# Optimization experiments

Hardware: AMD Instinct MI355X
Metric: run time of the kernel (lower is better)

The kernel has to match this reference:

```python
import jax, jax.numpy as jnp
import numpy as np

BN_EPS = 1e-5
RENORM_EPS = 1e-9


def setup_inputs() -> dict:
    key = jax.random.key(0)
    ks = jax.random.split(key, 8)
    B, C, N = 4, 256, 4096
    D = C // 4
    return {
        "x": jax.random.normal(ks[0], (B, C, N), jnp.float32),
        "y": jax.random.normal(ks[1], (B, C, N), jnp.float32),
        "w_qkx": jax.random.normal(ks[2], (D, C), jnp.float32) / np.sqrt(C),
        "w_vx": jax.random.normal(ks[3], (C, C), jnp.float32) / np.sqrt(C),
        "w_tx": jax.random.normal(ks[4], (C, C), jnp.float32) / np.sqrt(C),
        "w_qky": jax.random.normal(ks[5], (D, C), jnp.float32) / np.sqrt(C),
        "w_vy": jax.random.normal(ks[6], (C, C), jnp.float32) / np.sqrt(C),
        "w_ty": jax.random.normal(ks[7], (C, C), jnp.float32) / np.sqrt(C),
        "gamma": jnp.ones((C,), jnp.float32),
        "beta": jnp.zeros((C,), jnp.float32),
    }


def _conv1x1(w, x):
    # w: (O, C), x: (B, C, N) -> (B, O, N)
    return jnp.einsum("oc,bcn->bon", w, x)


def _batchnorm1d(x, gamma, beta):
    # training-mode BN over (B, N) per channel, biased variance (torch default)
    mean = x.mean(axis=(0, 2), keepdims=True)
    var = ((x - mean) ** 2).mean(axis=(0, 2), keepdims=True)
    xhat = (x - mean) * jax.lax.rsqrt(var + BN_EPS)
    return gamma[None, :, None] * xhat + beta[None, :, None]


def _branch(src, tgt, w_qk, w_v, w_t, gamma, beta):
    # cross-attention: queries from tgt, keys/values from src; output length = len(tgt)
    q = _conv1x1(w_qk, tgt)          # (B, D, M)
    k = _conv1x1(w_qk, src)          # (B, D, N)
    v = _conv1x1(w_v, src)           # (B, C, N)
    energy = jnp.einsum("bdm,bdn->bmn", q, k)      # (B, M, N)
    att = jax.nn.softmax(energy, axis=-1)
    att = att / (RENORM_EPS + att.sum(axis=2, keepdims=True))  # extra L1 renorm
    r = jnp.einsum("bcn,bmn->bcm", v, att)         # (B, C, M)
    return jax.nn.relu(_batchnorm1d(_conv1x1(w_t, r), gamma, beta))


def reference(x, y, w_qkx, w_vx, w_tx, w_qky, w_vy, w_ty, gamma, beta):
    r_x = _branch(x, y, w_qkx, w_vx, w_tx, gamma, beta)  # queries from y, kv from x
    r_y = _branch(y, x, w_qky, w_vy, w_ty, gamma, beta)  # queries from x, kv from y
    return (x + r_x, y + r_y)
```

## Files before the change

kernel.cpp:

```cpp
#include <hip/hip_runtime.h>

constexpr int Bc = 4;
constexpr int Cc = 256;
constexpr int Dc = 64;
constexpr int Nc = 4096;

typedef __attribute__((ext_vector_type(8))) _Float16 f16x8;
typedef __attribute__((ext_vector_type(4))) _Float16 f16x4;
typedef __attribute__((ext_vector_type(4))) float f32x4;

__device__ inline float exp2fast(float x) { return __builtin_amdgcn_exp2f(x); }

__device__ inline void gload_lds16(const _Float16* g, _Float16* lds) {
  __builtin_amdgcn_global_load_lds(
      (const __attribute__((address_space(1))) unsigned int*)g,
      (__attribute__((address_space(3))) unsigned int*)lds, 16, 0, 0);
}

__global__ __launch_bounds__(256) void wconv_kernel(
    const float* __restrict__ Wvx, const float* __restrict__ Wvy,
    const float* __restrict__ Wtx, const float* __restrict__ Wty,
    const float* __restrict__ Wqkx, const float* __restrict__ Wqky,
    _Float16* __restrict__ Wh)
{
  const int i = blockIdx.x * 256 + threadIdx.x;
  const int z = blockIdx.y;
  if (z < 4) {
    const float* w = (z == 0) ? Wvx : (z == 1) ? Wvy : (z == 2) ? Wtx : Wty;
    Wh[(size_t)z * Cc * Cc + i] = (_Float16)w[i];
  } else if (i < Dc * Cc) {
    const float* w = (z == 4) ? Wqkx : Wqky;
    Wh[(size_t)4 * Cc * Cc + (size_t)(z - 4) * Dc * Cc + i] = (_Float16)w[i];
  }
}

__global__ __launch_bounds__(256) void transpose_kernel(
    const float* __restrict__ X, const float* __restrict__ Y,
    _Float16* __restrict__ Xt)
{
  __shared__ float tile[64][65];
  const int t  = threadIdx.x;
  const int n0 = blockIdx.x * 64;
  const int c0 = blockIdx.y * 64;
  const int z  = blockIdx.z, br = z >> 2, b = z & 3;
  const float* In = (br ? Y : X) + (size_t)b * Cc * Nc;
#pragma unroll
  for (int p = 0; p < 4; ++p) {
    const int c = p * 16 + (t >> 4), n4 = (t & 15) * 4;
    float4 v = *(const float4*)&In[(size_t)(c0 + c) * Nc + n0 + n4];
    tile[c][n4 + 0] = v.x; tile[c][n4 + 1] = v.y;
    tile[c][n4 + 2] = v.z; tile[c][n4 + 3] = v.w;
  }
  __syncthreads();
  _Float16* Ob = Xt + ((size_t)(br * Bc + b) * Nc + n0) * Cc + c0;
#pragma unroll
  for (int p = 0; p < 4; ++p) {
    const int n = p * 16 + (t >> 4), c4 = (t & 15) * 4;
    f16x4 w;
#pragma unroll
    for (int j = 0; j < 4; ++j) w[j] = (_Float16)tile[c4 + j][n];
    *(f16x4*)&Ob[(size_t)n * Cc + c4] = w;
  }
}

__global__ __launch_bounds__(256, 4) void conv_qk_mfma_kernel(
    const _Float16* __restrict__ Xt, const _Float16* __restrict__ Wh,
    _Float16* __restrict__ Qt, _Float16* __restrict__ Kt)
{
  const int t  = threadIdx.x;
  const int ws = t >> 6, l = t & 63, lr = l & 15, lg = l >> 4;
  const int n_w = blockIdx.x * 128 + ws * 32;
  const int qk = blockIdx.y;
  const int z  = blockIdx.z, br = z >> 2, b = z & 3;
  const size_t bb = (size_t)(br * Bc + b);
  const int insel = (qk ^ br ^ 1) & 1;
  _Float16* Out = qk ? Kt : Qt;
  const float scale = qk ? 1.0f : 1.44269504088896f;

  const _Float16* wbase = Wh + (size_t)4 * Cc * Cc + (size_t)br * Dc * Cc
                          + (size_t)lr * Cc + lg * 8;
  const _Float16* xbase = Xt + ((size_t)(insel * Bc + b) * Nc + n_w + lr) * Cc + lg * 8;

  f32x4 acc[4][2] = {};
  for (int c0 = 0; c0 < Cc; c0 += 32) {
    f16x8 wf[4], xf[2];
#pragma unroll
    for (int dt = 0; dt < 4; ++dt)
      wf[dt] = *(const f16x8*)(wbase + (size_t)(dt * 16) * Cc + c0);
#pragma unroll
    for (int nt = 0; nt < 2; ++nt)
      xf[nt] = *(const f16x8*)(xbase + (size_t)(nt * 16) * Cc + c0);
#pragma unroll
    for (int dt = 0; dt < 4; ++dt)
#pragma unroll
      for (int nt = 0; nt < 2; ++nt)
        acc[dt][nt] = __builtin_amdgcn_mfma_f32_16x16x32_f16(wf[dt], xf[nt], acc[dt][nt], 0, 0, 0);
  }
#pragma unroll
  for (int dt = 0; dt < 4; ++dt)
#pragma unroll
    for (int nt = 0; nt < 2; ++nt) {
      const int n  = n_w + nt * 16 + lr;
      const int d0 = dt * 16 + lg * 4;
      const int off = qk ? (d0 ^ ((n & 7) << 3)) : d0;
      f16x4 o4;
#pragma unroll
      for (int r = 0; r < 4; ++r) o4[r] = (_Float16)(acc[dt][nt][r] * scale);
      *(f16x4*)&Out[(bb * Nc + n) * 64 + off] = o4;
    }
}

__global__ __launch_bounds__(256, 4) void conv_v_mfma_kernel(
    const _Float16* __restrict__ Xt, const _Float16* __restrict__ Wh,
    _Float16* __restrict__ Vb)
{
  const int t  = threadIdx.x;
  const int ws = t >> 6, l = t & 63, lr = l & 15, lg = l >> 4;
  const int wm = ws >> 1, wo = ws & 1;
  const int n_w = blockIdx.x * 128 + wm * 64;
  const int o_w = blockIdx.y * 128 + wo * 64;
  const int z  = blockIdx.z, br = z >> 2, b = z & 3;
  const size_t bb = (size_t)(br * Bc + b);

  const _Float16* abase = Xt + (bb * Nc + n_w + lr) * Cc + lg * 8;
  const _Float16* bbase = Wh + ((size_t)br * Cc + o_w + lr) * Cc + lg * 8;
  f32x4 acc[4][4] = {};

  for (int c0 = 0; c0 < Cc; c0 += 32) {
    f16x8 af[4], bfr[4];
#pragma unroll
    for (int mt = 0; mt < 4; ++mt)
      af[mt] = *(const f16x8*)(abase + (size_t)(mt * 16) * Cc + c0);
#pragma unroll
    for (int ot = 0; ot < 4; ++ot)
      bfr[ot] = *(const f16x8*)(bbase + (size_t)(ot * 16) * Cc + c0);
#pragma unroll
    for (int ot = 0; ot < 4; ++ot)
#pragma unroll
      for (int mt = 0; mt < 4; ++mt)
        acc[ot][mt] = __builtin_amdgcn_mfma_f32_16x16x32_f16(af[mt], bfr[ot], acc[ot][mt], 0, 0, 0);
  }
#pragma unroll
  for (int ot = 0; ot < 4; ++ot)
#pragma unroll
    for (int mt = 0; mt < 4; ++mt) {
      const int cout = o_w + ot * 16 + lr;
      const int n = n_w + mt * 16 + lg * 4;
      f16x4 o4;
#pragma unroll
      for (int r = 0; r < 4; ++r) o4[r] = (_Float16)acc[ot][mt][r];
      *(f16x4*)&Vb[(bb * Cc + cout) * Nc + n] = o4;
    }
}

__global__ __launch_bounds__(768, 3) void attn_mfma_kernel(
    const _Float16* __restrict__ Qt,
    const _Float16* __restrict__ Kt,
    const _Float16* __restrict__ V,
    _Float16* __restrict__ Op,
    float* __restrict__ Ml,
    int nsp, int kn)
{
  __shared__ __align__(16) _Float16 k_lds[2][64 * 64];
  __shared__ __align__(16) _Float16 p_lds[2][64 * 64];
  __shared__ float s_fac[2][64];

  const int t  = threadIdx.x;
  const int ws = t >> 6;
  const int l  = t & 63;
  const int lr = l & 15;
  const int lg = l >> 4;

  const int nwg  = (Nc / 64) * nsp * 8;
  const int lin  = blockIdx.x + gridDim.x * (blockIdx.y + gridDim.y * blockIdx.z);
  const int work = (lin & 7) * (nwg >> 3) + (lin >> 3);
  const int m0   = (work & 63) * 64;
  const int spbb = work >> 6;
  const int sp   = spbb % nsp;
  const size_t bb = (size_t)(spbb / nsp);

  const _Float16* kgl = Kt + (bb * Nc + (size_t)sp * kn) * 64;
  const int nch = kn >> 6;

  if (ws < 4) {
    const _Float16* qp = Qt + (bb * Nc + m0 + ws * 16 + lr) * 64 + lg * 8;
    const f16x8 qf0 = *(const f16x8*)qp;
    const f16x8 qf1 = *(const f16x8*)(qp + 32);
    const _Float16* gq = kgl + ws * 512 + l * 8;

    float m_run = -1e30f, l_run = 0.f;
    const int mrow = ws * 16 + lr;
    const int sw   = (mrow & 7) << 4;

    {
#pragma unroll
      for (int r = 0; r < 2; ++r)
        gload_lds16(gq + r * 2048, &k_lds[0][ws * 512 + r * 2048]);
    }
    __syncthreads();

    for (int ch2 = 0; ch2 < nch; ch2 += 2) {
#pragma unroll
      for (int par = 0; par < 2; ++par) {
        const int ch = ch2 + par;
        if (ch + 1 < nch) {
          const _Float16* g = gq + (size_t)(ch + 1) * (64 * 64);
#pragma unroll
          for (int r = 0; r < 2; ++r)
            gload_lds16(g + r * 2048, &k_lds[par ^ 1][ws * 512 + r * 2048]);
        }
        f32x4 st[4] = {};
#pragma unroll
        for (int nt = 0; nt < 4; ++nt) {
          const int   krow = nt * 16 + lr;
          const char* krp  = (const char*)&k_lds[par][krow * 64];
          const int   swr  = (krow & 7) << 4;
          f16x8 kh0 = *(const f16x8*)(krp + ((lg * 16) ^ swr));
          f16x8 kh1 = *(const f16x8*)(krp + ((64 + lg * 16) ^ swr));
          st[nt] = __builtin_amdgcn_mfma_f32_16x16x32_f16(kh0, qf0, st[nt], 0, 0, 0);
          st[nt] = __builtin_amdgcn_mfma_f32_16x16x32_f16(kh1, qf1, st[nt], 0, 0, 0);
        }
        float mx = st[0][0];
#pragma unroll
        for (int nt = 0; nt < 4; ++nt)
#pragma unroll
          for (int rr = 0; rr < 4; ++rr) mx = fmaxf(mx, st[nt][rr]);
        float s = 1.0f;
        if (__any(mx > m_run + 12.0f)) {
          mx = fmaxf(mx, __shfl_xor(mx, 16));
          mx = fmaxf(mx, __shfl_xor(mx, 32));
          const float mnew = fmaxf(m_run, mx);
          s = exp2fast(m_run - mnew);
          m_run = mnew;
        }
        float sum = 0.f;
        float p[4][4];
#pragma unroll
        for (int nt = 0; nt < 4; ++nt)
#pragma unroll
          for (int rr = 0; rr < 4; ++rr) {
            p[nt][rr] = exp2fast(st[nt][rr] - m_run);
            sum += p[nt][rr];
          }
        l_run = l_run * s + sum;
        {
          char* prow = (char*)&p_lds[par][mrow * 64];
#pragma unroll
          for (int nt = 0; nt < 4; ++nt) {
            f16x4 pb;
            pb[0] = (_Float16)p[nt][0]; pb[1] = (_Float16)p[nt][1];
            pb[2] = (_Float16)p[nt][2]; pb[3] = (_Float16)p[nt][3];
            *(f16x4*)(prow + ((nt * 32 + lg * 8) ^ sw)) = pb;
          }
        }
        if (lg == 0) s_fac[par][ws * 16 + lr] = s;
        __syncthreads();
      }
    }

    l_run += __shfl_xor(l_run, 16);
    l_run += __shfl_xor(l_run, 32);
    if (lg == 0) {
      size_t mi = ((bb * nsp + sp) * Nc + m0 + ws * 16 + lr) * 2;
      Ml[mi]     = m_run;
      Ml[mi + 1] = l_run;
    }
  } else {
    const int cw = ws - 4;
    const _Float16* vbase = V + (bb * Cc + cw * 32 + lr) * Nc + sp * kn + lg * 8;
    f32x4 acc[2][4] = {};
    f16x8 vf[2][2][2];

    __syncthreads();

    for (int ch2 = 0; ch2 < nch; ch2 += 2) {
#pragma unroll
      for (int par = 0; par < 2; ++par) {
        const int ch = ch2 + par;
        {
          const _Float16* vp = vbase + ch * 64;
#pragma unroll
          for (int ct = 0; ct < 2; ++ct)
#pragma unroll
            for (int kk = 0; kk < 2; ++kk)
              vf[par][ct][kk] = *(const f16x8*)(vp + (size_t)ct * 16 * Nc + kk * 32);
        }
        if (ch > 0) {
          float scm[4];
#pragma unroll
          for (int mt = 0; mt < 4; ++mt) scm[mt] = s_fac[par ^ 1][mt * 16 + lr];
          const int needs = (scm[0] != 1.f) | (scm[1] != 1.f) |
                            (scm[2] != 1.f) | (scm[3] != 1.f);
          if (__any(needs)) {
#pragma unroll
            for (int ct = 0; ct < 2; ++ct)
#pragma unroll
              for (int mt = 0; mt < 4; ++mt) {
                acc[ct][mt][0] *= scm[mt]; acc[ct][mt][1] *= scm[mt];
                acc[ct][mt][2] *= scm[mt]; acc[ct][mt][3] *= scm[mt];
              }
          }
          f16x8 pf[4][2];
#pragma unroll
          for (int mt = 0; mt < 4; ++mt) {
            const int   rm  = mt * 16 + lr;
            const char* pr  = (const char*)&p_lds[par ^ 1][rm * 64];
            const int   swr = (rm & 7) << 4;
#pragma unroll
            for (int kk = 0; kk < 2; ++kk)
              pf[mt][kk] = *(const f16x8*)(pr + ((lg * 16 + kk * 64) ^ swr));
          }
          __builtin_amdgcn_s_setprio(1);
#pragma unroll
          for (int ct = 0; ct < 2; ++ct)
#pragma unroll
            for (int kk = 0; kk < 2; ++kk)
#pragma unroll
              for (int mt = 0; mt < 4; ++mt)
                acc[ct][mt] = __builtin_amdgcn_mfma_f32_16x16x32_f16(vf[par ^ 1][ct][kk], pf[mt][kk], acc[ct][mt], 0, 0, 0);
          __builtin_amdgcn_s_setprio(0);
        }
        __syncthreads();
      }
    }

    {
      float scm[4];
#pragma unroll
      for (int mt = 0; mt < 4; ++mt) scm[mt] = s_fac[1][mt * 16 + lr];
      const int needs = (scm[0] != 1.f) | (scm[1] != 1.f) |
                        (scm[2] != 1.f) | (scm[3] != 1.f);
      if (__any(needs)) {
#pragma unroll
        for (int ct = 0; ct < 2; ++ct)
#pragma unroll
          for (int mt = 0; mt < 4; ++mt) {
            acc[ct][mt][0] *= scm[mt]; acc[ct][mt][1] *= scm[mt];
            acc[ct][mt][2] *= scm[mt]; acc[ct][mt][3] *= scm[mt];
          }
      }
      f16x8 pf[4][2];
#pragma unroll
      for (int mt = 0; mt < 4; ++mt) {
        const int   rm  = mt * 16 + lr;
        const char* pr  = (const char*)&p_lds[1][rm * 64];
        const int   swr = (rm & 7) << 4;
#pragma unroll
        for (int kk = 0; kk < 2; ++kk)
          pf[mt][kk] = *(const f16x8*)(pr + ((lg * 16 + kk * 64) ^ swr));
      }
#pragma unroll
      for (int ct = 0; ct < 2; ++ct)
#pragma unroll
        for (int kk = 0; kk < 2; ++kk)
#pragma unroll
          for (int mt = 0; mt < 4; ++mt)
            acc[ct][mt] = __builtin_amdgcn_mfma_f32_16x16x32_f16(vf[1][ct][kk], pf[mt][kk], acc[ct][mt], 0, 0, 0);
    }

    _Float16* ob = Op + (bb * nsp + sp) * (size_t)Cc * Nc;
#pragma unroll
    for (int ct = 0; ct < 2; ++ct)
#pragma unroll
      for (int mt = 0; mt < 4; ++mt) {
        const int c0 = cw * 32 + ct * 16 + lg * 4;
        const int m  = m0 + mt * 16 + lr;
        f16x4 o4;
#pragma unroll
        for (int r = 0; r < 4; ++r) o4[r] = (_Float16)acc[ct][mt][r];
        *(f16x4*)&ob[(size_t)m * Cc + c0] = o4;
      }
  }
}

__global__ __launch_bounds__(256) void combine_kernel(
    const _Float16* __restrict__ Op, const float* __restrict__ Ml,
    _Float16* __restrict__ Rt, int nsp)
{
  const int tid = blockIdx.x * 256 + threadIdx.x;
  const int c0 = (tid & 63) * 4;
  const int m  = (tid >> 6) & (Nc - 1);
  const int bb = tid >> 18;
  float val[4];
  if (nsp == 2) {
    const _Float16* o0 = Op + ((size_t)bb * 2 + 0) * Cc * Nc + (size_t)m * Cc + c0;
    const _Float16* o1 = Op + ((size_t)bb * 2 + 1) * Cc * Nc + (size_t)m * Cc + c0;
    const float* ml0 = Ml + (((size_t)bb * 2 + 0) * Nc + m) * 2;
    const float* ml1 = Ml + (((size_t)bb * 2 + 1) * Nc + m) * 2;
    float m1 = ml0[0], L1 = ml0[1], m2 = ml1[0], L2 = ml1[1];
    float M  = fmaxf(m1, m2);
    float w1 = __builtin_amdgcn_exp2f(m1 - M), w2 = __builtin_amdgcn_exp2f(m2 - M);
    float inv = 1.0f / (w1 * L1 + w2 * L2);
    f16x4 a = *(const f16x4*)o0;
    f16x4 d = *(const f16x4*)o1;
#pragma unroll
    for (int j = 0; j < 4; ++j) val[j] = (w1 * (float)a[j] + w2 * (float)d[j]) * inv;
  } else {
    const _Float16* o0 = Op + (size_t)bb * Cc * Nc + (size_t)m * Cc + c0;
    const float* ml0 = Ml + ((size_t)bb * Nc + m) * 2;
    float inv = 1.0f / ml0[1];
    f16x4 a = *(const f16x4*)o0;
#pragma unroll
    for (int j = 0; j < 4; ++j) val[j] = (float)a[j] * inv;
  }
  f16x4 r4;
#pragma unroll
  for (int j = 0; j < 4; ++j) r4[j] = (_Float16)val[j];
  *(f16x4*)&Rt[((size_t)bb * Nc + m) * Cc + c0] = r4;
}

__global__ __launch_bounds__(256, 4) void conv_t_mfma_kernel(
    const _Float16* __restrict__ Rt, const _Float16* __restrict__ Wh,
    _Float16* __restrict__ Th, float* __restrict__ part)
{
  __shared__ float red[2][2][4][16][2];
  const int t  = threadIdx.x;
  const int ws = t >> 6, l = t & 63, lr = l & 15, lg = l >> 4;
  const int wm = ws >> 1, wo = ws & 1;
  const int m_w = blockIdx.x * 128 + wm * 64;
  const int o_w = blockIdx.y * 128 + wo * 64;
  const int z  = blockIdx.z, br = z >> 2, b = z & 3;
  const size_t bb = (size_t)(br * Bc + b);

  const _Float16* abase = Rt + (bb * Nc + m_w + lr) * Cc + lg * 8;
  const _Float16* bbase = Wh + ((size_t)(2 + br) * Cc + o_w + lr) * Cc + lg * 8;
  f32x4 acc[4][4] = {};

  for (int c0 = 0; c0 < Cc; c0 += 32) {
    f16x8 af[4], bfr[4];
#pragma unroll
    for (int mt = 0; mt < 4; ++mt)
      af[mt] = *(const f16x8*)(abase + (size_t)(mt * 16) * Cc + c0);
#pragma unroll
    for (int ot = 0; ot < 4; ++ot)
      bfr[ot] = *(const f16x8*)(bbase + (size_t)(ot * 16) * Cc + c0);
#pragma unroll
    for (int ot = 0; ot < 4; ++ot)
#pragma unroll
      for (int mt = 0; mt < 4; ++mt)
        acc[ot][mt] = __builtin_amdgcn_mfma_f32_16x16x32_f16(af[mt], bfr[ot], acc[ot][mt], 0, 0, 0);
  }
  _Float16* Tb = Th + bb * Cc * Nc;
#pragma unroll
  for (int ot = 0; ot < 4; ++ot) {
    float s = 0.f, q = 0.f;
#pragma unroll
    for (int mt = 0; mt < 4; ++mt) {
      const int o = o_w + ot * 16 + lr;
      const int m = m_w + mt * 16 + lg * 4;
      f16x4 h4;
#pragma unroll
      for (int r = 0; r < 4; ++r) {
        float v = acc[ot][mt][r];
        h4[r] = (_Float16)v;
        s += v; q += v * v;
      }
      *(f16x4*)&Tb[(size_t)o * Nc + m] = h4;
    }
    s += __shfl_xor(s, 16); s += __shfl_xor(s, 32);
    q += __shfl_xor(q, 16); q += __shfl_xor(q, 32);
    if (lg == 0) { red[wm][wo][ot][lr][0] = s; red[wm][wo][ot][lr][1] = q; }
  }
  __syncthreads();
  {
    const int wo2 = t >> 7, ot2 = (t >> 5) & 3, lr2 = (t >> 1) & 15, kind = t & 1;
    float v = red[0][wo2][ot2][lr2][kind] + red[1][wo2][ot2][lr2][kind];
    const int c = blockIdx.y * 128 + wo2 * 64 + ot2 * 16 + lr2;
    const int slot = blockIdx.x * 4 + b;
    part[(((size_t)br * Cc + c) * 128 + slot) * 2 + kind] = v;
  }
}

__global__ __launch_bounds__(256) void bn_finalize_kernel(
    const float* __restrict__ part, float* __restrict__ stats)
{
  const int br = blockIdx.x, c = threadIdx.x;
  const float* p = part + ((size_t)br * Cc + c) * 128 * 2;
  float s = 0.f, q = 0.f;
#pragma unroll 4
  for (int i = 0; i < 128; ++i) { s += p[i * 2]; q += p[i * 2 + 1]; }
  const float inv_n = 1.0f / (float)(Bc * Nc);
  const float mean = s * inv_n;
  const float var  = q * inv_n - mean * mean;
  stats[(br * 2 + 0) * Cc + c] = mean;
  stats[(br * 2 + 1) * Cc + c] = rsqrtf(var + 1e-5f);
}

__global__ __launch_bounds__(256) void bn_out_kernel(
    const _Float16* __restrict__ Th, float* __restrict__ OUT,
    const float* __restrict__ X, const float* __restrict__ Y,
    const float* __restrict__ stats, const float* __restrict__ gamma,
    const float* __restrict__ beta)
{
  const int br = blockIdx.y;
  const int i = blockIdx.x * 256 + threadIdx.x;
  const size_t flat = ((size_t)i << 2);
  const int c = (int)((flat >> 12) & (Cc - 1));
  float mean = stats[(br * 2 + 0) * Cc + c], istd = stats[(br * 2 + 1) * Cc + c];
  float gm = gamma[c], bt = beta[c];
  const _Float16* Tb = Th + (size_t)br * Bc * Cc * Nc;
  float* Ob = OUT + (size_t)br * Bc * Cc * Nc;
  const float* SRC = (br ? Y : X);
  f16x4 t4 = *(const f16x4*)&Tb[flat];
  float4 s4 = *(const float4*)&SRC[flat];
  float4 o4;
  o4.x = s4.x + fmaxf(0.f, gm * ((float)t4[0] - mean) * istd + bt);
  o4.y = s4.y + fmaxf(0.f, gm * ((float)t4[1] - mean) * istd + bt);
  o4.z = s4.z + fmaxf(0.f, gm * ((float)t4[2] - mean) * istd + bt);
  o4.w = s4.w + fmaxf(0.f, gm * ((float)t4[3] - mean) * istd + bt);
  *(float4*)&Ob[flat] = o4;
}

extern "C" void kernel_launch(void* const* d_in, const int* in_sizes, int n_in,
                              void* d_out, int out_size, void* d_ws, size_t ws_size,
                              hipStream_t stream) {
  const float* x     = (const float*)d_in[0];
  const float* y     = (const float*)d_in[1];
  const float* w_qkx = (const float*)d_in[2];
  const float* w_vx  = (const float*)d_in[3];
  const float* w_tx  = (const float*)d_in[4];
  const float* w_qky = (const float*)d_in[5];
  const float* w_vy  = (const float*)d_in[6];
  const float* w_ty  = (const float*)d_in[7];
  const float* gamma = (const float*)d_in[8];
  const float* beta  = (const float*)d_in[9];

  float* out = (float*)d_out;

  const int nsp = (ws_size >= 60ull * 1024 * 1024) ? 2 : 1;
  const int kn  = Nc / nsp;

  char* wsb = (char*)d_ws;
  _Float16* qt = (_Float16*)wsb;
  _Float16* kt = (_Float16*)(wsb + (4ull << 20));
  _Float16* vb = (_Float16*)(wsb + (8ull << 20));
  _Float16* xt = (_Float16*)(wsb + (24ull << 20));
  _Float16* op = (_Float16*)(wsb + (24ull << 20));
  size_t off = (24ull << 20) + (size_t)nsp * (16ull << 20);
  float* ml = (float*)(wsb + off);
  off += (size_t)nsp * (256ull << 10);
  _Float16* wh = (_Float16*)(wsb + off);
  off += (640ull << 10);
  float* part = (float*)(wsb + off);
  off += (512ull << 10);
  float* st = (float*)(wsb + off);
  _Float16* rt = (_Float16*)wsb;
  _Float16* th = (_Float16*)(wsb + (24ull << 20));

  wconv_kernel<<<dim3(Cc * Cc / 256, 6), 256, 0, stream>>>(w_vx, w_vy, w_tx, w_ty, w_qkx, w_qky, wh);
  transpose_kernel<<<dim3(Nc / 64, Cc / 64, 8), 256, 0, stream>>>(x, y, xt);
  conv_qk_mfma_kernel<<<dim3(Nc / 128, 2, 8), 256, 0, stream>>>(xt, wh, qt, kt);
  conv_v_mfma_kernel<<<dim3(Nc / 128, Cc / 128, 8), 256, 0, stream>>>(xt, wh, vb);
  attn_mfma_kernel<<<dim3(Nc / 64, nsp, 8), 768, 0, stream>>>(qt, kt, vb, op, ml, nsp, kn);
  combine_kernel<<<(2 * Bc * Nc * (Cc / 4)) / 256, 256, 0, stream>>>(op, ml, rt, nsp);
  conv_t_mfma_kernel<<<dim3(Nc / 128, Cc / 128, 8), 256, 0, stream>>>(rt, wh, th, part);
  bn_finalize_kernel<<<2, 256, 0, stream>>>(part, st);
  bn_out_kernel<<<dim3((Bc * Cc * Nc / 4) / 256, 2), 256, 0, stream>>>(th, out, x, y, st, gamma, beta);
}
```

Baseline: 244.6 us.

## Triple-buffer K tiles with prefetch depth two and manual barriers

After: 266.8 us. 1.09x slower.

```diff
diff --git a/kernel.cpp b/kernel.cpp
--- a/kernel.cpp
+++ b/kernel.cpp
@@ -161,7 +161,7 @@
     float* __restrict__ Ml,
     int nsp, int kn)
 {
-  __shared__ __align__(16) _Float16 k_lds[2][64 * 64];
+  __shared__ __align__(16) _Float16 k_lds[3][64 * 64];
   __shared__ __align__(16) _Float16 p_lds[2][64 * 64];
   __shared__ float s_fac[2][64];
 
@@ -196,66 +196,79 @@
 #pragma unroll
       for (int r = 0; r < 2; ++r)
         gload_lds16(gq + r * 2048, &k_lds[0][ws * 512 + r * 2048]);
-    }
-    __syncthreads();
-
-    for (int ch2 = 0; ch2 < nch; ch2 += 2) {
-#pragma unroll
-      for (int par = 0; par < 2; ++par) {
-        const int ch = ch2 + par;
-        if (ch + 1 < nch) {
-          const _Float16* g = gq + (size_t)(ch + 1) * (64 * 64);
-#pragma unroll
-          for (int r = 0; r < 2; ++r)
-            gload_lds16(g + r * 2048, &k_lds[par ^ 1][ws * 512 + r * 2048]);
+#pragma unroll
+      for (int r = 0; r < 2; ++r)
+        gload_lds16(gq + (64 * 64) + r * 2048, &k_lds[1][ws * 512 + r * 2048]);
+      asm volatile("s_waitcnt vmcnt(2)" ::: "memory");
+    }
+    __builtin_amdgcn_s_barrier();
+    __builtin_amdgcn_sched_barrier(0);
+
+    int cur = 0;
+    for (int ch = 0; ch < nch; ++ch) {
+      const int par = ch & 1;
+      const bool more = (ch + 2 < nch);
+      if (more) {
+        int stg = cur + 2; if (stg >= 3) stg -= 3;
+        const _Float16* g = gq + (size_t)(ch + 2) * (64 * 64);
+#pragma unroll
+        for (int r = 0; r < 2; ++r)
+          gload_lds16(g + r * 2048, &k_lds[stg][ws * 512 + r * 2048]);
+      }
+      const _Float16* kbuf = &k_lds[cur][0];
+      f32x4 st[4] = {};
+#pragma unroll
+      for (int nt = 0; nt < 4; ++nt) {
+        const int   krow = nt * 16 + lr;
+        const char* krp  = (const char*)(kbuf + krow * 64);
+        const int   swr  = (krow & 7) << 4;
+        f16x8 kh0 = *(const f16x8*)(krp + ((lg * 16) ^ swr));
+        f16x8 kh1 = *(const f16x8*)(krp + ((64 + lg * 16) ^ swr));
+        st[nt] = __builtin_amdgcn_mfma_f32_16x16x32_f16(kh0, qf0, st[nt], 0, 0, 0);
+        st[nt] = __builtin_amdgcn_mfma_f32_16x16x32_f16(kh1, qf1, st[nt], 0, 0, 0);
+      }
+      float mx = st[0][0];
+#pragma unroll
+      for (int nt = 0; nt < 4; ++nt)
+#pragma unroll
+        for (int rr = 0; rr < 4; ++rr) mx = fmaxf(mx, st[nt][rr]);
+      float s = 1.0f;
+      if (__any(mx > m_run + 12.0f)) {
+        mx = fmaxf(mx, __shfl_xor(mx, 16));
+        mx = fmaxf(mx, __shfl_xor(mx, 32));
+        const float mnew = fmaxf(m_run, mx);
+        s = exp2fast(m_run - mnew);
+        m_run = mnew;
+      }
+      float sum = 0.f;
+      float p[4][4];
+#pragma unroll
+      for (int nt = 0; nt < 4; ++nt)
+#pragma unroll
+        for (int rr = 0; rr < 4; ++rr) {
+          p[nt][rr] = exp2fast(st[nt][rr] - m_run);
+          sum += p[nt][rr];
         }
-        f32x4 st[4] = {};
+      l_run = l_run * s + sum;
+      {
+        char* prow = (char*)&p_lds[par][mrow * 64];
 #pragma unroll
         for (int nt = 0; nt < 4; ++nt) {
-          const int   krow = nt * 16 + lr;
-          const char* krp  = (const char*)&k_lds[par][krow * 64];
-          const int   swr  = (krow & 7) << 4;
-          f16x8 kh0 = *(const f16x8*)(krp + ((lg * 16) ^ swr));
-          f16x8 kh1 = *(const f16x8*)(krp + ((64 + lg * 16) ^ swr));
-          st[nt] = __builtin_amdgcn_mfma_f32_16x16x32_f16(kh0, qf0, st[nt], 0, 0, 0);
-          st[nt] = __builtin_amdgcn_mfma_f32_16x16x32_f16(kh1, qf1, st[nt], 0, 0, 0);
+          f16x4 pb;
+          pb[0] = (_Float16)p[nt][0]; pb[1] = (_Float16)p[nt][1];
+          pb[2] = (_Float16)p[nt][2]; pb[3] = (_Float16)p[nt][3];
+          *(f16x4*)(prow + ((nt * 32 + lg * 8) ^ sw)) = pb;
         }
-        float mx = st[0][0];
-#pragma unroll
-        for (int nt = 0; nt < 4; ++nt)
-#pragma unroll
-          for (int rr = 0; rr < 4; ++rr) mx = fmaxf(mx, st[nt][rr]);
-        float s = 1.0f;
-        if (__any(mx > m_run + 12.0f)) {
-          mx = fmaxf(mx, __shfl_xor(mx, 16));
-          mx = fmaxf(mx, __shfl_xor(mx, 32));
-          const float mnew = fmaxf(m_run, mx);
-          s = exp2fast(m_run - mnew);
-          m_run = mnew;
-        }
-        float sum = 0.f;
-        float p[4][4];
-#pragma unroll
-        for (int nt = 0; nt < 4; ++nt)
-#pragma unroll
-          for (int rr = 0; rr < 4; ++rr) {
-            p[nt][rr] = exp2fast(st[nt][rr] - m_run);
-            sum += p[nt][rr];
-          }
-        l_run = l_run * s + sum;
-        {
-          char* prow = (char*)&p_lds[par][mrow * 64];
-#pragma unroll
-          for (int nt = 0; nt < 4; ++nt) {
-            f16x4 pb;
-            pb[0] = (_Float16)p[nt][0]; pb[1] = (_Float16)p[nt][1];
-            pb[2] = (_Float16)p[nt][2]; pb[3] = (_Float16)p[nt][3];
-            *(f16x4*)(prow + ((nt * 32 + lg * 8) ^ sw)) = pb;
-          }
-        }
-        if (lg == 0) s_fac[par][ws * 16 + lr] = s;
-        __syncthreads();
-      }
+      }
+      if (lg == 0) s_fac[par][ws * 16 + lr] = s;
+      if (more) {
+        asm volatile("s_waitcnt vmcnt(2) lgkmcnt(0)" ::: "memory");
+      } else {
+        asm volatile("s_waitcnt vmcnt(0) lgkmcnt(0)" ::: "memory");
+      }
+      __builtin_amdgcn_s_barrier();
+      __builtin_amdgcn_sched_barrier(0);
+      cur = (cur + 1 == 3) ? 0 : cur + 1;
     }
 
     l_run += __shfl_xor(l_run, 16);
@@ -271,7 +284,8 @@
     f32x4 acc[2][4] = {};
     f16x8 vf[2][2][2];
 
-    __syncthreads();
+    __builtin_amdgcn_s_barrier();
+    __builtin_amdgcn_sched_barrier(0);
 
     for (int ch2 = 0; ch2 < nch; ch2 += 2) {
 #pragma unroll
@@ -320,7 +334,9 @@
                 acc[ct][mt] = __builtin_amdgcn_mfma_f32_16x16x32_f16(vf[par ^ 1][ct][kk], pf[mt][kk], acc[ct][mt], 0, 0, 0);
           __builtin_amdgcn_s_setprio(0);
         }
-        __syncthreads();
+        asm volatile("s_waitcnt lgkmcnt(0)" ::: "memory");
+        __builtin_amdgcn_s_barrier();
+        __builtin_amdgcn_sched_barrier(0);
       }
     }
 
```

## Drop split-K attention and fuse softmax normalization into attention epilogue

Applied to the files above, without the earlier changes.

After: 230.4 us. -5.8%, faster.

```diff
diff --git a/kernel.cpp b/kernel.cpp
--- a/kernel.cpp
+++ b/kernel.cpp
@@ -157,9 +157,7 @@
     const _Float16* __restrict__ Qt,
     const _Float16* __restrict__ Kt,
     const _Float16* __restrict__ V,
-    _Float16* __restrict__ Op,
-    float* __restrict__ Ml,
-    int nsp, int kn)
+    _Float16* __restrict__ Rt)
 {
   __shared__ __align__(16) _Float16 k_lds[2][64 * 64];
   __shared__ __align__(16) _Float16 p_lds[2][64 * 64];
@@ -171,16 +169,14 @@
   const int lr = l & 15;
   const int lg = l >> 4;
 
-  const int nwg  = (Nc / 64) * nsp * 8;
-  const int lin  = blockIdx.x + gridDim.x * (blockIdx.y + gridDim.y * blockIdx.z);
+  const int nwg  = (Nc / 64) * 8;
+  const int lin  = blockIdx.x + gridDim.x * blockIdx.z;
   const int work = (lin & 7) * (nwg >> 3) + (lin >> 3);
   const int m0   = (work & 63) * 64;
-  const int spbb = work >> 6;
-  const int sp   = spbb % nsp;
-  const size_t bb = (size_t)(spbb / nsp);
-
-  const _Float16* kgl = Kt + (bb * Nc + (size_t)sp * kn) * 64;
-  const int nch = kn >> 6;
+  const size_t bb = (size_t)(work >> 6);
+
+  const _Float16* kgl = Kt + bb * Nc * 64;
+  const int nch = Nc >> 6;
 
   if (ws < 4) {
     const _Float16* qp = Qt + (bb * Nc + m0 + ws * 16 + lr) * 64 + lg * 8;
@@ -260,14 +256,11 @@
 
     l_run += __shfl_xor(l_run, 16);
     l_run += __shfl_xor(l_run, 32);
-    if (lg == 0) {
-      size_t mi = ((bb * nsp + sp) * Nc + m0 + ws * 16 + lr) * 2;
-      Ml[mi]     = m_run;
-      Ml[mi + 1] = l_run;
-    }
+    if (lg == 0) s_fac[0][mrow] = l_run;
+    __syncthreads();
   } else {
     const int cw = ws - 4;
-    const _Float16* vbase = V + (bb * Cc + cw * 32 + lr) * Nc + sp * kn + lg * 8;
+    const _Float16* vbase = V + (bb * Cc + cw * 32 + lr) * Nc + lg * 8;
     f32x4 acc[2][4] = {};
     f16x8 vf[2][2][2];
 
@@ -358,7 +351,12 @@
             acc[ct][mt] = __builtin_amdgcn_mfma_f32_16x16x32_f16(vf[1][ct][kk], pf[mt][kk], acc[ct][mt], 0, 0, 0);
     }
 
-    _Float16* ob = Op + (bb * nsp + sp) * (size_t)Cc * Nc;
+    __syncthreads();
+
+    float linv[4];
+#pragma unroll
+    for (int mt = 0; mt < 4; ++mt) linv[mt] = 1.0f / s_fac[0][mt * 16 + lr];
+    _Float16* ob = Rt + bb * (size_t)Nc * Cc;
 #pragma unroll
     for (int ct = 0; ct < 2; ++ct)
 #pragma unroll
@@ -367,46 +365,10 @@
         const int m  = m0 + mt * 16 + lr;
         f16x4 o4;
 #pragma unroll
-        for (int r = 0; r < 4; ++r) o4[r] = (_Float16)acc[ct][mt][r];
+        for (int r = 0; r < 4; ++r) o4[r] = (_Float16)(acc[ct][mt][r] * linv[mt]);
         *(f16x4*)&ob[(size_t)m * Cc + c0] = o4;
       }
   }
-}
-
-__global__ __launch_bounds__(256) void combine_kernel(
-    const _Float16* __restrict__ Op, const float* __restrict__ Ml,
-    _Float16* __restrict__ Rt, int nsp)
-{
-  const int tid = blockIdx.x * 256 + threadIdx.x;
-  const int c0 = (tid & 63) * 4;
-  const int m  = (tid >> 6) & (Nc - 1);
-  const int bb = tid >> 18;
-  float val[4];
-  if (nsp == 2) {
-    const _Float16* o0 = Op + ((size_t)bb * 2 + 0) * Cc * Nc + (size_t)m * Cc + c0;
-    const _Float16* o1 = Op + ((size_t)bb * 2 + 1) * Cc * Nc + (size_t)m * Cc + c0;
-    const float* ml0 = Ml + (((size_t)bb * 2 + 0) * Nc + m) * 2;
-    const float* ml1 = Ml + (((size_t)bb * 2 + 1) * Nc + m) * 2;
-    float m1 = ml0[0], L1 = ml0[1], m2 = ml1[0], L2 = ml1[1];
-    float M  = fmaxf(m1, m2);
-    float w1 = __builtin_amdgcn_exp2f(m1 - M), w2 = __builtin_amdgcn_exp2f(m2 - M);
-    float inv = 1.0f / (w1 * L1 + w2 * L2);
-    f16x4 a = *(const f16x4*)o0;
-    f16x4 d = *(const f16x4*)o1;
-#pragma unroll
-    for (int j = 0; j < 4; ++j) val[j] = (w1 * (float)a[j] + w2 * (float)d[j]) * inv;
-  } else {
-    const _Float16* o0 = Op + (size_t)bb * Cc * Nc + (size_t)m * Cc + c0;
-    const float* ml0 = Ml + ((size_t)bb * Nc + m) * 2;
-    float inv = 1.0f / ml0[1];
-    f16x4 a = *(const f16x4*)o0;
-#pragma unroll
-    for (int j = 0; j < 4; ++j) val[j] = (float)a[j] * inv;
-  }
-  f16x4 r4;
-#pragma unroll
-  for (int j = 0; j < 4; ++j) r4[j] = (_Float16)val[j];
-  *(f16x4*)&Rt[((size_t)bb * Nc + m) * Cc + c0] = r4;
 }
 
 __global__ __launch_bounds__(256, 4) void conv_t_mfma_kernel(
@@ -527,32 +489,22 @@
 
   float* out = (float*)d_out;
 
-  const int nsp = (ws_size >= 60ull * 1024 * 1024) ? 2 : 1;
-  const int kn  = Nc / nsp;
-
   char* wsb = (char*)d_ws;
   _Float16* qt = (_Float16*)wsb;
   _Float16* kt = (_Float16*)(wsb + (4ull << 20));
   _Float16* vb = (_Float16*)(wsb + (8ull << 20));
   _Float16* xt = (_Float16*)(wsb + (24ull << 20));
-  _Float16* op = (_Float16*)(wsb + (24ull << 20));
-  size_t off = (24ull << 20) + (size_t)nsp * (16ull << 20);
-  float* ml = (float*)(wsb + off);
-  off += (size_t)nsp * (256ull << 10);
-  _Float16* wh = (_Float16*)(wsb + off);
-  off += (640ull << 10);
-  float* part = (float*)(wsb + off);
-  off += (512ull << 10);
-  float* st = (float*)(wsb + off);
-  _Float16* rt = (_Float16*)wsb;
-  _Float16* th = (_Float16*)(wsb + (24ull << 20));
+  _Float16* rt = (_Float16*)(wsb + (24ull << 20));
+  _Float16* th = (_Float16*)(wsb + (40ull << 20));
+  _Float16* wh = (_Float16*)(wsb + (56ull << 20));
+  float* part  = (float*)(wsb + (56ull << 20) + (640ull << 10));
+  float* st    = (float*)(wsb + (56ull << 20) + (1152ull << 10));
 
   wconv_kernel<<<dim3(Cc * Cc / 256, 6), 256, 0, stream>>>(w_vx, w_vy, w_tx, w_ty, w_qkx, w_qky, wh);
   transpose_kernel<<<dim3(Nc / 64, Cc / 64, 8), 256, 0, stream>>>(x, y, xt);
   conv_qk_mfma_kernel<<<dim3(Nc / 128, 2, 8), 256, 0, stream>>>(xt, wh, qt, kt);
   conv_v_mfma_kernel<<<dim3(Nc / 128, Cc / 128, 8), 256, 0, stream>>>(xt, wh, vb);
-  attn_mfma_kernel<<<dim3(Nc / 64, nsp, 8), 768, 0, stream>>>(qt, kt, vb, op, ml, nsp, kn);
-  combine_kernel<<<(2 * Bc * Nc * (Cc / 4)) / 256, 256, 0, stream>>>(op, ml, rt, nsp);
+  attn_mfma_kernel<<<dim3(Nc / 64, 1, 8), 768, 0, stream>>>(qt, kt, vb, rt);
   conv_t_mfma_kernel<<<dim3(Nc / 128, Cc / 128, 8), 256, 0, stream>>>(rt, wh, th, part);
   bn_finalize_kernel<<<2, 256, 0, stream>>>(part, st);
   bn_out_kernel<<<dim3((Bc * Cc * Nc / 4) / 256, 2), 256, 0, stream>>>(th, out, x, y, st, gamma, beta);
```
